# Optimization experiments

Measured on AMD Instinct MI355X. Metric: run time of the kernel, lower is better.

## Reference

```python
import jax, jax.numpy as jnp
import numpy as np
from jax import lax

CANTOR_DEPTH = 8
VOCAB, D = 100000, 128


def setup_inputs() -> dict:
    key = jax.random.key(0)
    pentachora = jax.random.normal(key, (VOCAB, 5, D), dtype=jnp.float32)
    return {"pentachora": pentachora}


def _cantor_positions(V):
    # V: [N, 5, D]
    dt = V.dtype
    diff = V[:, :, None, :] - V[:, None, :, :]          # [N,5,5,D]
    dist_sq = jnp.sum(diff * diff, axis=-1)             # [N,5,5]
    N = V.shape[0]

    # Batched 6x6 Cayley-Menger matrix
    M = jnp.zeros((N, 6, 6), dtype=dt)
    M = M.at[:, 0, 1:].set(1.0)
    M = M.at[:, 1:, 0].set(1.0)
    M = M.at[:, 1:, 1:].set(dist_sq)
    det = jnp.linalg.det(M)                              # [N]
    volume = jnp.sqrt(jnp.clip(-det / 9216.0, 0.0))

    # Edge statistics over the 10 unique edges (torch .std() uses ddof=1)
    iu, ju = np.triu_indices(5, k=1)
    edge_lengths = jnp.sqrt(dist_sq[:, iu, ju])          # [N,10]
    mean_edge = jnp.mean(edge_lengths, axis=-1)
    std_edge = jnp.std(edge_lengths, axis=-1, ddof=1)

    # Vertex spread from centroid (ddof=1)
    centroid = jnp.mean(V, axis=1, keepdims=True)        # [N,1,D]
    cdist = jnp.linalg.norm(V - centroid, axis=-1)       # [N,5]
    spread = jnp.std(cdist, axis=-1, ddof=1)

    volume_norm = jax.nn.sigmoid(volume * 10.0)
    edge_ratio = jax.nn.sigmoid(std_edge / (mean_edge + 1e-6))
    spread_norm = jax.nn.sigmoid(spread)

    seed = jnp.clip(volume_norm * 0.4 + edge_ratio * 0.3 + spread_norm * 0.3,
                    1e-6, 1.0 - 1e-6)
    drift = (volume_norm + edge_ratio + spread_norm) * 0.01

    def step(carry, factor):
        x, cv = carry
        x_scaled = x * 3.0
        digit = jnp.floor(x_scaled)                      # x>0 so floor==trunc
        x_frac = x_scaled - digit
        cv = cv + (digit == 2.0).astype(dt) * factor
        x = jnp.clip(x_frac + drift, 1e-6, 1.0 - 1e-6)
        return (x, cv), None

    factors = (0.5 ** jnp.arange(1, CANTOR_DEPTH + 1)).astype(dt)
    (_, cantor_val), _ = lax.scan(step, (seed, jnp.zeros_like(seed)), factors)
    return jnp.clip(cantor_val, 0.0, 1.0)                # [N]


def reference(pentachora):
    return _cantor_positions(pentachora)
```

## Files before the change

kernel.cpp:

```cpp
#include <hip/hip_runtime.h>
#include <math.h>


typedef float f32x4 __attribute__((ext_vector_type(4)));

__device__ __forceinline__ constexpr int gidx(int i, int j) {
    return i * 5 - i * (i - 1) / 2 + (j - i);
}

__global__ __launch_bounds__(256, 4) void fingerprint_kernel(
    const float* __restrict__ pent, float* __restrict__ out, int nItems)
{
    __shared__ double lds_g[32][15];

    const int tid  = threadIdx.x;
    const int wave = tid >> 6;
    const int lane = tid & 63;
    const int grp  = lane >> 3;
    const int s    = lane & 7;

    long item  = (long)blockIdx.x * 32 + (long)wave * 8 + grp;
    long itemC = item < nItems ? item : (long)nItems - 1;

    const f32x4* __restrict__ p =
        reinterpret_cast<const f32x4*>(pent + itemC * 640L);

    f32x4 f[5][4];
#pragma unroll
    for (int v = 0; v < 5; ++v)
#pragma unroll
        for (int j = 0; j < 4; ++j)
            f[v][j] = __builtin_nontemporal_load(&p[v * 32 + j * 8 + s]);

    const float* fp = reinterpret_cast<const float*>(f);

    double g[15];
#pragma unroll
    for (int q = 0; q < 15; ++q) g[q] = 0.0;

#pragma unroll
    for (int t = 0; t < 16; ++t) {
        double a[5];
#pragma unroll
        for (int v = 0; v < 5; ++v)
            a[v] = (double)fp[v * 16 + t];
        int q = 0;
#pragma unroll
        for (int i = 0; i < 5; ++i)
#pragma unroll
            for (int j = i; j < 5; ++j) {
                g[q] = fma(a[i], a[j], g[q]);
                ++q;
            }
    }

#pragma unroll
    for (int m = 1; m <= 4; m <<= 1)
#pragma unroll
        for (int q = 0; q < 15; ++q) g[q] += __shfl_xor(g[q], m, 64);

    if (s == 0) {
        const int slot = wave * 8 + grp;
#pragma unroll
        for (int q = 0; q < 15; ++q) lds_g[slot][q] = g[q];
    }
    __syncthreads();

    if (tid < 32) {
        const long item2 = (long)blockIdx.x * 32 + tid;

        double h[15];
#pragma unroll
        for (int q = 0; q < 15; ++q) h[q] = lds_g[tid][q];

        double e[10];
        double se = 0.0;
        {
            int q = 0;
#pragma unroll
            for (int i = 0; i < 5; ++i)
#pragma unroll
                for (int j = i + 1; j < 5; ++j) {
                    double d2 = fma(-2.0, h[gidx(i, j)],
                                    h[gidx(i, i)] + h[gidx(j, j)]);
                    e[q] = sqrt(d2);
                    se += e[q];
                    ++q;
                }
        }
        double meanE = se * 0.1;
        double ve = 0.0;
#pragma unroll
        for (int q = 0; q < 10; ++q) {
            double d = e[q] - meanE;
            ve = fma(d, d, ve);
        }
        double stdE = sqrt(ve / 9.0);

        double S[5], T = 0.0;
#pragma unroll
        for (int i = 0; i < 5; ++i) {
            double si = 0.0;
#pragma unroll
            for (int j = 0; j < 5; ++j) {
                int a = i < j ? i : j;
                int b = i < j ? j : i;
                si += h[gidx(a, b)];
            }
            S[i] = si;
            T += si;
        }

        double scd = 0.0, cd[5];
#pragma unroll
        for (int v = 0; v < 5; ++v) {
            double c2 = fma(-0.4, S[v], h[gidx(v, v)]) + 0.04 * T;
            cd[v] = (c2 > 0.0) ? sqrt(c2) : 0.0;
            scd += cd[v];
        }
        double meanC = scd * 0.2;
        double vc = 0.0;
#pragma unroll
        for (int v = 0; v < 5; ++v) {
            double d = cd[v] - meanC;
            vc = fma(d, d, vc);
        }
        double spread = sqrt(vc * 0.25);

        double W[4][4];
#pragma unroll
        for (int pi = 0; pi < 4; ++pi)
#pragma unroll
            for (int qi = 0; qi < 4; ++qi) {
                int lo = (pi < qi ? pi : qi) + 1;
                int hi = (pi < qi ? qi : pi) + 1;
                W[pi][qi] = h[gidx(lo, hi)] - h[gidx(0, qi + 1)]
                          - h[gidx(0, pi + 1)] + h[gidx(0, 0)];
            }

        double det = 1.0;
#pragma unroll
        for (int k = 0; k < 4; ++k) {
            double pv = W[k][k];
            det *= pv;
            double inv = (pv != 0.0) ? 1.0 / pv : 0.0;
#pragma unroll
            for (int r = k + 1; r < 4; ++r) {
                double fac = W[r][k] * inv;
#pragma unroll
                for (int c = k + 1; c < 4; ++c)
                    W[r][c] = fma(-fac, W[k][c], W[r][c]);
            }
        }

        double v2 = det / 576.0;
        double volume = (v2 > 0.0) ? sqrt(v2) : 0.0;

        double vn = 1.0 / (1.0 + exp(-10.0 * volume));
        double er = 1.0 / (1.0 + exp(-(stdE / (meanE + 1e-6))));
        double sn = 1.0 / (1.0 + exp(-spread));

        double seed = 0.4 * vn + 0.3 * er + 0.3 * sn;
        seed = fmin(fmax(seed, 1e-6), 1.0 - 1e-6);
        double drift = (vn + er + sn) * 0.01;

        double x = seed, cv = 0.0, factor = 0.5;
#pragma unroll
        for (int k = 0; k < 8; ++k) {
            double xs = x * 3.0;
            double dg = floor(xs);
            double fr = xs - dg;
            cv += (dg == 2.0) ? factor : 0.0;
            factor *= 0.5;
            x = fmin(fmax(fr + drift, 1e-6), 1.0 - 1e-6);
        }
        cv = fmin(fmax(cv, 0.0), 1.0);

        if (item2 < nItems)
            __builtin_nontemporal_store((float)cv, &out[item2]);
    }
}

extern "C" void kernel_launch(void* const* d_in, const int* in_sizes, int n_in,
                              void* d_out, int out_size, void* d_ws, size_t ws_size,
                              hipStream_t stream) {
    const float* pent = (const float*)d_in[0];
    float* out = (float*)d_out;
    int nItems = in_sizes[0] / 640;
    int blocks = (nItems + 31) / 32;
    hipLaunchKernelGGL(fingerprint_kernel, dim3(blocks), dim3(256), 0, stream,
                       pent, out, nItems);
}
```

Measured before the change: 44.66 us.

## Process two item batches per block with recursive-halving shuffle reduction

```diff
diff --git a/kernel.cpp b/kernel.cpp
--- a/kernel.cpp
+++ b/kernel.cpp
@@ -11,67 +11,94 @@
 __global__ __launch_bounds__(256, 4) void fingerprint_kernel(
     const float* __restrict__ pent, float* __restrict__ out, int nItems)
 {
-    __shared__ double lds_g[32][15];
+    __shared__ double lds_g[16][64];
 
     const int tid  = threadIdx.x;
     const int wave = tid >> 6;
     const int lane = tid & 63;
     const int grp  = lane >> 3;
     const int s    = lane & 7;
-
-    long item  = (long)blockIdx.x * 32 + (long)wave * 8 + grp;
-    long itemC = item < nItems ? item : (long)nItems - 1;
-
-    const f32x4* __restrict__ p =
-        reinterpret_cast<const f32x4*>(pent + itemC * 640L);
-
-    f32x4 f[5][4];
-#pragma unroll
-    for (int v = 0; v < 5; ++v)
-#pragma unroll
-        for (int j = 0; j < 4; ++j)
-            f[v][j] = __builtin_nontemporal_load(&p[v * 32 + j * 8 + s]);
-
-    const float* fp = reinterpret_cast<const float*>(f);
-
-    double g[15];
-#pragma unroll
-    for (int q = 0; q < 15; ++q) g[q] = 0.0;
-
-#pragma unroll
-    for (int t = 0; t < 16; ++t) {
-        double a[5];
+    const int k = ((s & 1) << 3) | ((s & 2) << 1) | ((s & 4) >> 1);
+
+    const long base = (long)blockIdx.x * 64;
+
+#pragma unroll
+    for (int c = 0; c < 2; ++c) {
+        const int slot = c * 32 + wave * 8 + grp;
+        long item  = base + slot;
+        long itemC = item < nItems ? item : (long)nItems - 1;
+
+        const f32x4* __restrict__ p =
+            reinterpret_cast<const f32x4*>(pent + itemC * 640L);
+
+        f32x4 f[5][4];
 #pragma unroll
         for (int v = 0; v < 5; ++v)
-            a[v] = (double)fp[v * 16 + t];
-        int q = 0;
-#pragma unroll
-        for (int i = 0; i < 5; ++i)
-#pragma unroll
-            for (int j = i; j < 5; ++j) {
-                g[q] = fma(a[i], a[j], g[q]);
-                ++q;
-            }
+#pragma unroll
+            for (int j = 0; j < 4; ++j)
+                f[v][j] = __builtin_nontemporal_load(&p[v * 32 + j * 8 + s]);
+
+        const float* fp = reinterpret_cast<const float*>(f);
+
+        double g[16];
+#pragma unroll
+        for (int q = 0; q < 16; ++q) g[q] = 0.0;
+
+#pragma unroll
+        for (int t = 0; t < 16; ++t) {
+            double a[5];
+#pragma unroll
+            for (int v = 0; v < 5; ++v)
+                a[v] = (double)fp[v * 16 + t];
+            int q = 0;
+#pragma unroll
+            for (int i = 0; i < 5; ++i)
+#pragma unroll
+                for (int j = i; j < 5; ++j) {
+                    g[q] = fma(a[i], a[j], g[q]);
+                    ++q;
+                }
+        }
+
+        {
+            const bool b = (s & 1) != 0;
+#pragma unroll
+            for (int i = 0; i < 8; ++i) {
+                double lo = g[i], hi = g[i + 8];
+                double recv = __shfl_xor(b ? lo : hi, 1, 64);
+                g[i] = (b ? hi : lo) + recv;
+            }
+        }
+        {
+            const bool b = (s & 2) != 0;
+#pragma unroll
+            for (int i = 0; i < 4; ++i) {
+                double lo = g[i], hi = g[i + 4];
+                double recv = __shfl_xor(b ? lo : hi, 2, 64);
+                g[i] = (b ? hi : lo) + recv;
+            }
+        }
+        {
+            const bool b = (s & 4) != 0;
+#pragma unroll
+            for (int i = 0; i < 2; ++i) {
+                double lo = g[i], hi = g[i + 2];
+                double recv = __shfl_xor(b ? lo : hi, 4, 64);
+                g[i] = (b ? hi : lo) + recv;
+            }
+        }
+        lds_g[k][slot]     = g[0];
+        lds_g[k + 1][slot] = g[1];
     }
 
-#pragma unroll
-    for (int m = 1; m <= 4; m <<= 1)
-#pragma unroll
-        for (int q = 0; q < 15; ++q) g[q] += __shfl_xor(g[q], m, 64);
-
-    if (s == 0) {
-        const int slot = wave * 8 + grp;
-#pragma unroll
-        for (int q = 0; q < 15; ++q) lds_g[slot][q] = g[q];
-    }
     __syncthreads();
 
-    if (tid < 32) {
-        const long item2 = (long)blockIdx.x * 32 + tid;
+    if (tid < 64) {
+        const long item2 = base + tid;
 
         double h[15];
 #pragma unroll
-        for (int q = 0; q < 15; ++q) h[q] = lds_g[tid][q];
+        for (int q = 0; q < 15; ++q) h[q] = lds_g[q][tid];
 
         double e[10];
         double se = 0.0;
@@ -140,16 +167,16 @@
 
         double det = 1.0;
 #pragma unroll
-        for (int k = 0; k < 4; ++k) {
-            double pv = W[k][k];
+        for (int kk = 0; kk < 4; ++kk) {
+            double pv = W[kk][kk];
             det *= pv;
             double inv = (pv != 0.0) ? 1.0 / pv : 0.0;
 #pragma unroll
-            for (int r = k + 1; r < 4; ++r) {
-                double fac = W[r][k] * inv;
-#pragma unroll
-                for (int c = k + 1; c < 4; ++c)
-                    W[r][c] = fma(-fac, W[k][c], W[r][c]);
+            for (int r = kk + 1; r < 4; ++r) {
+                double fac = W[r][kk] * inv;
+#pragma unroll
+                for (int cc = kk + 1; cc < 4; ++cc)
+                    W[r][cc] = fma(-fac, W[kk][cc], W[r][cc]);
             }
         }
 
@@ -166,7 +193,7 @@
 
         double x = seed, cv = 0.0, factor = 0.5;
 #pragma unroll
-        for (int k = 0; k < 8; ++k) {
+        for (int kk = 0; kk < 8; ++kk) {
             double xs = x * 3.0;
             double dg = floor(xs);
             double fr = xs - dg;
@@ -187,7 +214,7 @@
     const float* pent = (const float*)d_in[0];
     float* out = (float*)d_out;
     int nItems = in_sizes[0] / 640;
-    int blocks = (nItems + 31) / 32;
+    int blocks = (nItems + 63) / 64;
     hipLaunchKernelGGL(fingerprint_kernel, dim3(blocks), dim3(256), 0, stream,
                        pent, out, nItems);
 }
```

New measurement: 160.3 us. 259% more time.
